# Optimization experiments

Hardware: AMD Instinct MI355X
Metric: run time of the kernel (lower is better)

## Reference

```python
import jax, jax.numpy as jnp
import numpy as np

T, IO, H, M = 8192, 32, 256, 4  # timesteps, io_width, hidden_width, max ponder steps
EPS = 0.01  # ACT halting epsilon


def setup_inputs() -> dict:
    key = jax.random.key(0)
    ks = jax.random.split(key, 8)
    sc = 0.05
    return {
        "x": jax.random.normal(ks[0], (T, IO), jnp.float32),
        "h0": jnp.zeros((H,), jnp.float32),                       # act1_h initial state
        "Wp": jax.random.normal(ks[1], (H, IO), jnp.float32) * sc,  # input_processing Linear
        "bp": jnp.zeros((H,), jnp.float32),
        "Wx": jax.random.normal(ks[2], (H, H + 1), jnp.float32) * sc,  # ACT cell input weights (+1 first-step flag)
        "Ws": jax.random.normal(ks[3], (H, H), jnp.float32) * sc,      # ACT cell recurrent weights
        "b": jnp.zeros((H,), jnp.float32),
        "wh": jax.random.normal(ks[4], (H,), jnp.float32) * sc,        # halting unit
        "bh": jnp.float32(1.0),
        "Wo": jax.random.normal(ks[5], (IO, H), jnp.float32) * sc,     # ACT output projection
        "bo": jnp.zeros((IO,), jnp.float32),
    }


def reference(x, h0, Wp, bp, Wx, Ws, b, wh, bh, Wo, bo):
    # Faithful translation: per-timestep loop (lax.scan) over the sequence; each step
    # runs input_processing then an ACT (Graves) ponder loop with max M=4 steps.
    # io_noise is identity in eval mode. attention_beam_width=1 => line == current point.
    T_ = x.shape[0]

    def step(carry, x_t):
        h, pc = carry
        lin1 = Wp @ x_t + bp  # [H]
        s = h
        cum = jnp.float32(0.0)
        acc_s = jnp.zeros_like(h)
        acc_y = jnp.zeros_like(bo)
        n_up = jnp.float32(0.0)
        rem = jnp.float32(0.0)
        still = jnp.bool_(True)
        for n in range(M):  # fixed small ponder loop, masked ACT halting
            flag = jnp.full((1,), 1.0 if n == 0 else 0.0, lin1.dtype)
            inp = jnp.concatenate([lin1, flag])  # [H+1]
            s = jnp.tanh(Wx @ inp + Ws @ s + b)
            p = jax.nn.sigmoid(wh @ s + bh)
            halt = (cum + p > 1.0 - EPS) | (n == M - 1)
            w = jnp.where(still, jnp.where(halt, 1.0 - cum, p), 0.0)
            acc_s = acc_s + w * s
            acc_y = acc_y + w * (Wo @ s + bo)
            rem = rem + jnp.where(still & halt, 1.0 - cum, 0.0)
            n_up = n_up + jnp.where(still, 1.0, 0.0)
            cum = cum + w
            still = still & jnp.logical_not(halt)
        ponder = n_up + rem  # N(t) + R(t)
        pc = (pc + ponder) / jnp.float32(T_)  # matches the in-loop division in the original forward
        return (acc_s, pc), acc_y

    (_, pc), ys = jax.lax.scan(step, (h0, jnp.float32(0.0)), x)
    return ys, pc
```

## Files before the change

kernel.cpp:

```cpp
#include <hip/hip_runtime.h>


#define T_  8192
#define IO_ 32
#define H_  256

typedef __attribute__((ext_vector_type(2))) float v2f;

template<int CTRL>
__device__ __forceinline__ float dpp_addf(float x) {
    int xi = __builtin_bit_cast(int, x);
    int d = __builtin_amdgcn_update_dpp(xi, xi, CTRL, 0xF, 0xF, false);
    return x + __builtin_bit_cast(float, d);
}
__device__ __forceinline__ void bar_lds() {
    asm volatile("s_waitcnt lgkmcnt(0)\n\ts_barrier" ::: "memory");
    __builtin_amdgcn_sched_barrier(0);
}

__global__ void k_prep(const float* __restrict__ Wx,
                       const float* __restrict__ Wp,
                       const float* __restrict__ bp,
                       const float* __restrict__ b,
                       float* __restrict__ WxpT, float* __restrict__ cvec) {
    int h = blockIdx.x;
    int t = threadIdx.x;
    __shared__ float wxrow[H_];
    for (int j = t; j < H_; j += 64) wxrow[j] = Wx[h * (H_ + 1) + j];
    __syncthreads();
    if (t < IO_) {
        float acc = 0.0f;
        for (int j = 0; j < H_; ++j) acc += wxrow[j] * Wp[j * IO_ + t];
        WxpT[t * H_ + h] = acc;
    } else if (t == IO_) {
        float acc = b[h];
        for (int j = 0; j < H_; ++j) acc += wxrow[j] * bp[j];
        cvec[h] = acc;
    }
}

__global__ void k_u(const float* __restrict__ x,
                    const float* __restrict__ WxpT,
                    const float* __restrict__ cvec,
                    float* __restrict__ U) {
    int t0 = blockIdx.x * 8;
    int tid = threadIdx.x;
    __shared__ float xsf[8 * IO_];
    xsf[tid] = x[(size_t)t0 * IO_ + tid];
    __syncthreads();
    int h = tid;
    float base = cvec[h];
    const float L2E2 = 2.8853900817779268f;
    for (int tt = 0; tt < 8; ++tt) {
        float acc = base;
        #pragma unroll
        for (int io = 0; io < IO_; ++io)
            acc += WxpT[io * H_ + h] * xsf[tt * IO_ + io];
        U[(size_t)(t0 + tt) * H_ + h] = acc * L2E2;
    }
}

__global__ __launch_bounds__(512, 2) void act_chain(
    const float* __restrict__ Ws,
    const float* __restrict__ Wx,
    const float* __restrict__ wh,
    const float* __restrict__ bh1,
    const float* __restrict__ h0,
    float* __restrict__ UAcc,
    float* __restrict__ cumArr,
    float* __restrict__ pc_out)
{
    __shared__ __align__(16) float sbuf[2][4 * 68];
    __shared__ __align__(16) float plds[2][8];

    const int tid = threadIdx.x;
    const int w   = tid >> 6;
    const int l   = tid & 63;
    const int rg  = l >> 2;
    const int c   = l & 3;
    const int rowbase = w * 32 + rg * 2;
    const int schunk  = rowbase >> 6;
    const int soff    = rowbase & 63;

    const float L2E  = 1.4426950408889634f;
    const float L2E2 = 2.8853900817779268f;

    v2f wt[2][32];
    #pragma unroll
    for (int r = 0; r < 2; ++r) {
        const float4* src = (const float4*)(Ws + (size_t)(rowbase + r) * H_ + c * 64);
        #pragma unroll
        for (int q = 0; q < 16; ++q) {
            float4 f = src[q];
            wt[r][2 * q]     = (v2f){f.x * L2E2, f.y * L2E2};
            wt[r][2 * q + 1] = (v2f){f.z * L2E2, f.w * L2E2};
        }
    }

    v2f wl2, whp2;
    wl2.x  = Wx[(size_t)rowbase * (H_ + 1) + H_] * L2E2;
    wl2.y  = Wx[(size_t)(rowbase + 1) * (H_ + 1) + H_] * L2E2;
    whp2.x = wh[rowbase]     * (-L2E);
    whp2.y = wh[rowbase + 1] * (-L2E);
    const float bhp = -bh1[0] * L2E;
    const float thresh = 1.0f - 0.01f;

    auto matvec = [&](const float4* sp) -> v2f {
        v2f a0[4] = {{0.f,0.f},{0.f,0.f},{0.f,0.f},{0.f,0.f}};
        v2f a1[4] = {{0.f,0.f},{0.f,0.f},{0.f,0.f},{0.f,0.f}};
        #pragma unroll
        for (int q = 0; q < 16; ++q) {
            float4 f = sp[q];
            v2f sa = (v2f){f.x, f.y};
            v2f sb = (v2f){f.z, f.w};
            a0[q & 1]       = a0[q & 1]       + wt[0][2 * q]     * sa;
            a0[2 + (q & 1)] = a0[2 + (q & 1)] + wt[0][2 * q + 1] * sb;
            a1[q & 1]       = a1[q & 1]       + wt[1][2 * q]     * sa;
            a1[2 + (q & 1)] = a1[2 + (q & 1)] + wt[1][2 * q + 1] * sb;
        }
        v2f t0 = (a0[0] + a0[1]) + (a0[2] + a0[3]);
        v2f t1 = (a1[0] + a1[1]) + (a1[2] + a1[3]);
        float y0 = t0.x + t0.y;
        float y1 = t1.x + t1.y;
        y0 = dpp_addf<0xB1>(y0); y0 = dpp_addf<0x4E>(y0);
        y1 = dpp_addf<0xB1>(y1); y1 = dpp_addf<0x4E>(y1);
        return (v2f){y0, y1};
    };

    v2f zh;
    {
        float4 hbuf[16];
        const float4* hp = (const float4*)(h0 + c * 64);
        #pragma unroll
        for (int q = 0; q < 16; ++q) hbuf[q] = hp[q];
        zh = matvec(hbuf);
    }

    float pc = 0.0f;
    v2f un  = *(const v2f*)(UAcc + rowbase);
    v2f un1 = *(const v2f*)(UAcc + (T_ > 1 ? H_ : 0) + rowbase);
    v2f uw0 = un + wl2;

    auto round = [&](int WB, int PP, v2f in, v2f& z, float& p) -> v2f {
        float e0 = __builtin_amdgcn_exp2f(in.x);
        float e1 = __builtin_amdgcn_exp2f(in.y);
        float s0 = __builtin_fmaf(-2.0f, __builtin_amdgcn_rcpf(e0 + 1.0f), 1.0f);
        float s1 = __builtin_fmaf(-2.0f, __builtin_amdgcn_rcpf(e1 + 1.0f), 1.0f);
        if (c == 0) *(v2f*)(&sbuf[WB][schunk * 68 + soff]) = (v2f){s0, s1};
        float part = __builtin_fmaf(whp2.x, s0, whp2.y * s1);
        part = dpp_addf<0x124>(part);
        part = dpp_addf<0x128>(part);
        part = dpp_addf<0x142>(part);
        part = dpp_addf<0x143>(part);
        if (l == 63) plds[PP][w] = part;
        bar_lds();
        float4 pa = *(const float4*)(&plds[PP][0]);
        float4 pb = *(const float4*)(&plds[PP][4]);
        float dot = ((pa.x + pa.y) + (pa.z + pa.w)) +
                    ((pb.x + pb.y) + (pb.z + pb.w));
        p = __builtin_amdgcn_rcpf(1.0f + __builtin_amdgcn_exp2f(dot + bhp));
        z = matvec((const float4*)(&sbuf[WB][c * 68]));
        return (v2f){s0, s1};
    };

    #pragma unroll 1
    for (int t = 0; t < T_; ++t) {
        const int tn2 = (t + 2 < T_) ? t + 2 : T_ - 1;
        const v2f un2 = *(const v2f*)(UAcc + (size_t)tn2 * H_ + rowbase);

        v2f z0, z1;
        float p0, p1;
        v2f s0 = round(0, 0, zh + uw0, z0, p0);
        v2f s1 = round(1, 1, z0 + un,  z1, p1);

        bool  halt0  = p0 > thresh;
        float w0     = halt0 ? 1.0f : p0;
        bool  still1 = !halt0;
        float cum1   = w0;
        bool  halt1  = (cum1 + p1 > thresh);
        float w1     = still1 ? (halt1 ? 1.0f - cum1 : p1) : 0.0f;
        v2f   accs   = w0 * s0 + w1 * s1;
        v2f   zacc   = w0 * z0 + w1 * z1;
        float cum    = cum1 + w1;
        float nup    = still1 ? 2.0f : 1.0f;
        float rem    = halt0 ? 1.0f : (halt1 ? 1.0f - cum1 : 0.0f);

        if (still1 && !halt1) {
            v2f z2, z3;
            float p2, p3;
            v2f s2 = round(0, 0, z1 + un, z2, p2);
            bool  halt2 = (cum + p2 > thresh);
            float w2    = halt2 ? 1.0f - cum : p2;
            float rem2  = halt2 ? 1.0f - cum : 0.0f;
            accs = accs + w2 * s2;
            zacc = zacc + w2 * z2;
            float cum3   = cum + w2;
            bool  still3 = !halt2;
            v2f s3 = round(1, 1, z2 + un, z3, p3);
            float w3 = still3 ? (1.0f - cum3) : 0.0f;
            accs = accs + w3 * s3;
            zacc = zacc + w3 * z3;
            rem  = rem2 + w3;
            cum  = cum3 + w3;
            nup  = still3 ? 4.0f : 3.0f;
        }

        pc = (pc + nup + rem) * (1.0f / (float)T_);
        zh = zacc;
        if (c == 0) *(v2f*)(UAcc + (size_t)t * H_ + rowbase) = accs;
        if (tid == 0) cumArr[t] = cum;
        un  = un1;
        un1 = un2;
        uw0 = un + wl2;
    }
    if (tid == 0) pc_out[0] = pc;
}

__global__ void k_out(const float* __restrict__ AccS,
                      const float* __restrict__ Wo,
                      const float* __restrict__ bo,
                      const float* __restrict__ cumArr,
                      float* __restrict__ ys) {
    int t0 = blockIdx.x * 8;
    int tid = threadIdx.x;
    __shared__ float wo[IO_ * 257];
    __shared__ float as[8 * 260];
    for (int i = tid; i < IO_ * H_; i += 256) {
        int o = i / H_, h = i % H_;
        wo[o * 257 + h] = Wo[i];
    }
    for (int i = tid; i < 8 * H_; i += 256) {
        int tt = i / H_, h = i % H_;
        as[tt * 260 + h] = AccS[(size_t)t0 * H_ + i];
    }
    __syncthreads();
    int tt = tid >> 5, o = tid & 31;
    float acc = cumArr[t0 + tt] * bo[o];
    #pragma unroll 4
    for (int h = 0; h < H_; ++h) acc += wo[o * 257 + h] * as[tt * 260 + h];
    ys[(size_t)(t0 + tt) * IO_ + o] = acc;
}

extern "C" void kernel_launch(void* const* d_in, const int* in_sizes, int n_in,
                              void* d_out, int out_size, void* d_ws, size_t ws_size,
                              hipStream_t stream) {
    const float* x  = (const float*)d_in[0];
    const float* h0 = (const float*)d_in[1];
    const float* Wp = (const float*)d_in[2];
    const float* bp = (const float*)d_in[3];
    const float* Wx = (const float*)d_in[4];
    const float* Ws = (const float*)d_in[5];
    const float* b  = (const float*)d_in[6];
    const float* wh = (const float*)d_in[7];
    const float* bh = (const float*)d_in[8];
    const float* Wo = (const float*)d_in[9];
    const float* bo = (const float*)d_in[10];
    float* out = (float*)d_out;

    char* ws = (char*)d_ws;
    float* WxpT = (float*)ws;
    float* cvec = (float*)(ws + 32768);
    float* cumA = (float*)(ws + 33792);
    float* UAcc = (float*)(ws + 66560);

    k_prep<<<H_, 64, 0, stream>>>(Wx, Wp, bp, b, WxpT, cvec);
    k_u<<<T_ / 8, 256, 0, stream>>>(x, WxpT, cvec, UAcc);
    act_chain<<<1, 512, 0, stream>>>(Ws, Wx, wh, bh, h0, UAcc, cumA,
                                     out + (size_t)T_ * IO_);
    k_out<<<T_ / 8, 256, 0, stream>>>(UAcc, Wo, bo, cumA, out);
}
```

Baseline: 11.80 ms.

## Shrink serial ACT chain block to 4 waves with 4 rows per lane-group

The single-block recurrent kernel now runs 256 threads (4 waves) instead of 512, with each 4-lane group owning 4 hidden rows instead of 2. This doubles per-thread weight registers (128 floats of Ws) and matvec work, while halving the number of waves that must meet at each barrier and the partial sums combined for the halting dot. The aim is to shorten barrier and synchronisation latency on the serial per-step critical path, at the cost of more work per thread and higher register pressure.

```diff
diff --git a/kernel.cpp b/kernel.cpp
--- a/kernel.cpp
+++ b/kernel.cpp
@@ -6,6 +6,7 @@
 #define H_  256
 
 typedef __attribute__((ext_vector_type(2))) float v2f;
+typedef __attribute__((ext_vector_type(4))) float v4f;
 
 template<int CTRL>
 __device__ __forceinline__ float dpp_addf(float x) {
@@ -60,7 +61,7 @@
     }
 }
 
-__global__ __launch_bounds__(512, 2) void act_chain(
+__global__ __launch_bounds__(256, 1) void act_chain(
     const float* __restrict__ Ws,
     const float* __restrict__ Wx,
     const float* __restrict__ wh,
@@ -78,100 +79,108 @@
     const int l   = tid & 63;
     const int rg  = l >> 2;
     const int c   = l & 3;
-    const int rowbase = w * 32 + rg * 2;
-    const int schunk  = rowbase >> 6;
-    const int soff    = rowbase & 63;
+    const int rowbase = w * 64 + rg * 4;
+    const int pubidx = w * 68 + rg * 4;
 
     const float L2E  = 1.4426950408889634f;
     const float L2E2 = 2.8853900817779268f;
 
-    v2f wt[2][32];
+    v2f wt[4][32];
     #pragma unroll
-    for (int r = 0; r < 2; ++r) {
-        const float4* src = (const float4*)(Ws + (size_t)(rowbase + r) * H_ + c * 64);
+    for (int r = 0; r < 4; ++r) {
+        const v4f* src = (const v4f*)(Ws + (size_t)(rowbase + r) * H_ + c * 64);
         #pragma unroll
         for (int q = 0; q < 16; ++q) {
-            float4 f = src[q];
-            wt[r][2 * q]     = (v2f){f.x * L2E2, f.y * L2E2};
-            wt[r][2 * q + 1] = (v2f){f.z * L2E2, f.w * L2E2};
-        }
-    }
-
-    v2f wl2, whp2;
-    wl2.x  = Wx[(size_t)rowbase * (H_ + 1) + H_] * L2E2;
-    wl2.y  = Wx[(size_t)(rowbase + 1) * (H_ + 1) + H_] * L2E2;
-    whp2.x = wh[rowbase]     * (-L2E);
-    whp2.y = wh[rowbase + 1] * (-L2E);
+            v4f f = src[q];
+            wt[r][2 * q]     = (v2f){f[0] * L2E2, f[1] * L2E2};
+            wt[r][2 * q + 1] = (v2f){f[2] * L2E2, f[3] * L2E2};
+        }
+    }
+
+    v4f wl4, whp4;
+    #pragma unroll
+    for (int r = 0; r < 4; ++r) {
+        wl4[r]  = Wx[(size_t)(rowbase + r) * (H_ + 1) + H_] * L2E2;
+        whp4[r] = wh[rowbase + r] * (-L2E);
+    }
     const float bhp = -bh1[0] * L2E;
     const float thresh = 1.0f - 0.01f;
 
-    auto matvec = [&](const float4* sp) -> v2f {
-        v2f a0[4] = {{0.f,0.f},{0.f,0.f},{0.f,0.f},{0.f,0.f}};
-        v2f a1[4] = {{0.f,0.f},{0.f,0.f},{0.f,0.f},{0.f,0.f}};
+    auto matvec = [&](const v4f* sp) -> v4f {
+        v2f acc[4][4];
+        #pragma unroll
+        for (int r = 0; r < 4; ++r)
+            #pragma unroll
+            for (int a = 0; a < 4; ++a) acc[r][a] = (v2f){0.f, 0.f};
         #pragma unroll
         for (int q = 0; q < 16; ++q) {
-            float4 f = sp[q];
-            v2f sa = (v2f){f.x, f.y};
-            v2f sb = (v2f){f.z, f.w};
-            a0[q & 1]       = a0[q & 1]       + wt[0][2 * q]     * sa;
-            a0[2 + (q & 1)] = a0[2 + (q & 1)] + wt[0][2 * q + 1] * sb;
-            a1[q & 1]       = a1[q & 1]       + wt[1][2 * q]     * sa;
-            a1[2 + (q & 1)] = a1[2 + (q & 1)] + wt[1][2 * q + 1] * sb;
-        }
-        v2f t0 = (a0[0] + a0[1]) + (a0[2] + a0[3]);
-        v2f t1 = (a1[0] + a1[1]) + (a1[2] + a1[3]);
-        float y0 = t0.x + t0.y;
-        float y1 = t1.x + t1.y;
-        y0 = dpp_addf<0xB1>(y0); y0 = dpp_addf<0x4E>(y0);
-        y1 = dpp_addf<0xB1>(y1); y1 = dpp_addf<0x4E>(y1);
-        return (v2f){y0, y1};
+            v4f f = sp[q];
+            v2f sa = (v2f){f[0], f[1]};
+            v2f sb = (v2f){f[2], f[3]};
+            #pragma unroll
+            for (int r = 0; r < 4; ++r) {
+                acc[r][q & 1]       = acc[r][q & 1]       + wt[r][2 * q]     * sa;
+                acc[r][2 + (q & 1)] = acc[r][2 + (q & 1)] + wt[r][2 * q + 1] * sb;
+            }
+        }
+        v4f y;
+        #pragma unroll
+        for (int r = 0; r < 4; ++r) {
+            v2f t = (acc[r][0] + acc[r][1]) + (acc[r][2] + acc[r][3]);
+            float yy = t.x + t.y;
+            yy = dpp_addf<0xB1>(yy);
+            yy = dpp_addf<0x4E>(yy);
+            y[r] = yy;
+        }
+        return y;
     };
 
-    v2f zh;
+    v4f zh;
     {
-        float4 hbuf[16];
-        const float4* hp = (const float4*)(h0 + c * 64);
+        v4f hbuf[16];
+        const v4f* hp = (const v4f*)(h0 + c * 64);
         #pragma unroll
         for (int q = 0; q < 16; ++q) hbuf[q] = hp[q];
         zh = matvec(hbuf);
     }
 
     float pc = 0.0f;
-    v2f un  = *(const v2f*)(UAcc + rowbase);
-    v2f un1 = *(const v2f*)(UAcc + (T_ > 1 ? H_ : 0) + rowbase);
-    v2f uw0 = un + wl2;
-
-    auto round = [&](int WB, int PP, v2f in, v2f& z, float& p) -> v2f {
-        float e0 = __builtin_amdgcn_exp2f(in.x);
-        float e1 = __builtin_amdgcn_exp2f(in.y);
-        float s0 = __builtin_fmaf(-2.0f, __builtin_amdgcn_rcpf(e0 + 1.0f), 1.0f);
-        float s1 = __builtin_fmaf(-2.0f, __builtin_amdgcn_rcpf(e1 + 1.0f), 1.0f);
-        if (c == 0) *(v2f*)(&sbuf[WB][schunk * 68 + soff]) = (v2f){s0, s1};
-        float part = __builtin_fmaf(whp2.x, s0, whp2.y * s1);
+    v4f un  = *(const v4f*)(UAcc + rowbase);
+    v4f un1 = *(const v4f*)(UAcc + H_ + rowbase);
+    v4f uw0 = un + wl4;
+
+    auto round = [&](int WB, int PP, v4f in, v4f& z, float& p) -> v4f {
+        v4f s;
+        #pragma unroll
+        for (int i = 0; i < 4; ++i) {
+            float e = __builtin_amdgcn_exp2f(in[i]);
+            s[i] = __builtin_fmaf(-2.0f, __builtin_amdgcn_rcpf(e + 1.0f), 1.0f);
+        }
+        if (c == 0) *(v4f*)(&sbuf[WB][pubidx]) = s;
+        float part = (whp4[0] * s[0] + whp4[1] * s[1]) +
+                     (whp4[2] * s[2] + whp4[3] * s[3]);
         part = dpp_addf<0x124>(part);
         part = dpp_addf<0x128>(part);
         part = dpp_addf<0x142>(part);
         part = dpp_addf<0x143>(part);
         if (l == 63) plds[PP][w] = part;
         bar_lds();
-        float4 pa = *(const float4*)(&plds[PP][0]);
-        float4 pb = *(const float4*)(&plds[PP][4]);
-        float dot = ((pa.x + pa.y) + (pa.z + pa.w)) +
-                    ((pb.x + pb.y) + (pb.z + pb.w));
+        v4f pa = *(const v4f*)(&plds[PP][0]);
+        float dot = (pa[0] + pa[1]) + (pa[2] + pa[3]);
         p = __builtin_amdgcn_rcpf(1.0f + __builtin_amdgcn_exp2f(dot + bhp));
-        z = matvec((const float4*)(&sbuf[WB][c * 68]));
-        return (v2f){s0, s1};
+        z = matvec((const v4f*)(&sbuf[WB][c * 68]));
+        return s;
     };
 
     #pragma unroll 1
     for (int t = 0; t < T_; ++t) {
         const int tn2 = (t + 2 < T_) ? t + 2 : T_ - 1;
-        const v2f un2 = *(const v2f*)(UAcc + (size_t)tn2 * H_ + rowbase);
-
-        v2f z0, z1;
+        const v4f un2 = *(const v4f*)(UAcc + (size_t)tn2 * H_ + rowbase);
+
+        v4f z0, z1;
         float p0, p1;
-        v2f s0 = round(0, 0, zh + uw0, z0, p0);
-        v2f s1 = round(1, 1, z0 + un,  z1, p1);
+        v4f s0 = round(0, 0, zh + uw0, z0, p0);
+        v4f s1 = round(1, 1, z0 + un,  z1, p1);
 
         bool  halt0  = p0 > thresh;
         float w0     = halt0 ? 1.0f : p0;
@@ -179,16 +188,16 @@
         float cum1   = w0;
         bool  halt1  = (cum1 + p1 > thresh);
         float w1     = still1 ? (halt1 ? 1.0f - cum1 : p1) : 0.0f;
-        v2f   accs   = w0 * s0 + w1 * s1;
-        v2f   zacc   = w0 * z0 + w1 * z1;
+        v4f   accs   = w0 * s0 + w1 * s1;
+        v4f   zacc   = w0 * z0 + w1 * z1;
         float cum    = cum1 + w1;
         float nup    = still1 ? 2.0f : 1.0f;
         float rem    = halt0 ? 1.0f : (halt1 ? 1.0f - cum1 : 0.0f);
 
         if (still1 && !halt1) {
-            v2f z2, z3;
+            v4f z2, z3;
             float p2, p3;
-            v2f s2 = round(0, 0, z1 + un, z2, p2);
+            v4f s2 = round(0, 0, z1 + un, z2, p2);
             bool  halt2 = (cum + p2 > thresh);
             float w2    = halt2 ? 1.0f - cum : p2;
             float rem2  = halt2 ? 1.0f - cum : 0.0f;
@@ -196,7 +205,7 @@
             zacc = zacc + w2 * z2;
             float cum3   = cum + w2;
             bool  still3 = !halt2;
-            v2f s3 = round(1, 1, z2 + un, z3, p3);
+            v4f s3 = round(1, 1, z2 + un, z3, p3);
             float w3 = still3 ? (1.0f - cum3) : 0.0f;
             accs = accs + w3 * s3;
             zacc = zacc + w3 * z3;
@@ -207,11 +216,11 @@
 
         pc = (pc + nup + rem) * (1.0f / (float)T_);
         zh = zacc;
-        if (c == 0) *(v2f*)(UAcc + (size_t)t * H_ + rowbase) = accs;
+        if (c == 0) *(v4f*)(UAcc + (size_t)t * H_ + rowbase) = accs;
         if (tid == 0) cumArr[t] = cum;
         un  = un1;
         un1 = un2;
-        uw0 = un + wl2;
+        uw0 = un + wl4;
     }
     if (tid == 0) pc_out[0] = pc;
 }
@@ -265,7 +274,7 @@
 
     k_prep<<<H_, 64, 0, stream>>>(Wx, Wp, bp, b, WxpT, cvec);
     k_u<<<T_ / 8, 256, 0, stream>>>(x, WxpT, cvec, UAcc);
-    act_chain<<<1, 512, 0, stream>>>(Ws, Wx, wh, bh, h0, UAcc, cumA,
+    act_chain<<<1, 256, 0, stream>>>(Ws, Wx, wh, bh, h0, UAcc, cumA,
                                      out + (size_t)T_ * IO_);
     k_out<<<T_ / 8, 256, 0, stream>>>(UAcc, Wo, bo, cumA, out);
 }
```

Result: slower. 19.55 ms (+65.6%).
